# Performance work log

Hardware: AMD Instinct MI355X
Metric: run time of the kernel (lower is better)

Reference implementation:

```python
import jax, jax.numpy as jnp
import numpy as np

B = 131072   # batch (tokens)
D = 512      # d_model
P = 10       # n_programs
H = D // 4   # extractor hidden
MAXO = 4     # max operands
MAXR = 3     # max results


def setup_inputs() -> dict:
    key = jax.random.key(0)
    ks = jax.random.split(key, 6)
    hidden = jax.random.normal(ks[0], (B, D), jnp.float32)
    program_ids = jax.random.randint(ks[1], (B,), 0, P)
    Wr = jax.random.normal(ks[2], (D, P), jnp.float32) * (1.0 / np.sqrt(D))
    br = jnp.zeros((P,), jnp.float32)
    # stacked per-program extractor MLPs, output padded to MAXO (extra cols unused)
    W1 = jax.random.normal(ks[3], (P, D, H), jnp.float32) * (1.0 / np.sqrt(D))
    b1 = jnp.zeros((P, H), jnp.float32)
    W2 = jax.random.normal(ks[4], (P, H, MAXO), jnp.float32) * (1.0 / np.sqrt(H))
    b2 = jnp.zeros((P, MAXO), jnp.float32)
    return {"hidden": hidden, "program_ids": program_ids, "Wr": Wr, "br": br,
            "W1": W1, "b1": b1, "W2": W2, "b2": b2}


def _time_decompose(total_minutes):
    days = jnp.floor(total_minutes / 1440.0)
    rem = total_minutes - days * 1440.0
    hours = jnp.floor(rem / 60.0)
    minutes = rem - hours * 60.0
    return hours, minutes, days


def _safe(b):
    # avoid NaN/Inf from zero denominators in Mod/FloorDiv
    return jnp.where(b == 0, 1.0, b)


def _programs():
    # (fn -> tuple of result arrays, n_operands), order matches DEFAULT_PROGRAMS
    return [
        (lambda a, b: (a + b,), 2),                                   # IntAdd
        (lambda a, b: (a - b,), 2),                                   # IntSub
        (lambda a, b: (a * b,), 2),                                   # IntMul
        (lambda a, b: (jnp.mod(a, _safe(b)),), 2),                    # Mod
        (lambda a, b: (jnp.floor(a / _safe(b)),), 2),                 # FloorDiv
        (lambda h1, m1, h2, m2: _time_decompose(h1 * 60 + m1 + h2 * 60 + m2), 4),          # TimeAdd
        (lambda h1, m1, h2, m2: _time_decompose(h1 * 60 + m1 - (h2 * 60 + m2)), 4),        # TimeSub
        (lambda h1, m1, h2, m2: _time_decompose(jnp.abs(h1 * 60 + m1 - (h2 * 60 + m2))), 4),  # DurationBetween
        (lambda a, b: ((a > b).astype(jnp.float32),), 2),             # Greater
        (lambda a, b: ((a == b).astype(jnp.float32),), 2),            # Equal
    ]


def _compute_results(ops_rounded):
    # ops_rounded: [P, B, MAXO] -> results_all [P, B, MAXR]
    outs = []
    for idx, (fn, nop) in enumerate(_programs()):
        args = [ops_rounded[idx, :, i] for i in range(nop)]
        res = fn(*args)
        cols = list(res) + [jnp.zeros_like(res[0])] * (MAXR - len(res))
        outs.append(jnp.stack(cols, axis=-1))  # [B, MAXR]
    return jnp.stack(outs, axis=0)  # [P, B, MAXR]


def reference(hidden, program_ids, Wr, br, W1, b1, W2, b2):
    router_logits = hidden @ Wr + br                                  # [B, P]
    pre = jnp.einsum('bd,pdh->pbh', hidden, W1) + b1[:, None, :]      # [P, B, H]
    ops = jnp.einsum('pbh,pho->pbo', jax.nn.gelu(pre, approximate=False), W2) + b2[:, None, :]  # [P, B, MAXO]
    ops_rounded = jnp.round(ops)  # round_ste forward = round
    results_all = _compute_results(ops_rounded)                       # [P, B, MAXR]
    # combine: each row takes the result of its own program (masked scatter in torch)
    results = results_all[program_ids, jnp.arange(hidden.shape[0])]   # [B, MAXR]
    results = jax.lax.stop_gradient(results)  # torch .detach()
    return results, router_logits, ops, program_ids
```

## Files before the change

### kernel.cpp

```cpp
#include <hip/hip_runtime.h>
#include <math.h>

constexpr int D_   = 512;
constexpr int H_   = 128;
constexpr int P_   = 10;
constexpr int MAXO = 4;
constexpr int BM   = 128;
constexpr int BK   = 32;

typedef _Float16 f16;
typedef f16 f16x4 __attribute__((ext_vector_type(4)));
typedef f16 f16x8 __attribute__((ext_vector_type(8)));
typedef float f32x4 __attribute__((ext_vector_type(4)));

__device__ __forceinline__ float gelu_exact(float x) {
    return 0.5f * x * (1.0f + erff(x * 0.70710678118654752f));
}

__device__ __forceinline__ void time_decomp(float t, float& hr, float& mi, float& dy) {
    float days = floorf(t / 1440.0f);
    float rem  = t - days * 1440.0f;
    float hours = floorf(rem / 60.0f);
    float minutes = rem - hours * 60.0f;
    hr = hours; mi = minutes; dy = days;
}

__device__ __forceinline__ void g2l16(const f16* g, f16* l) {
    __builtin_amdgcn_global_load_lds(
        (const __attribute__((address_space(1))) void*)g,
        (__attribute__((address_space(3))) void*)l, 16, 0, 0);
}

__global__ __launch_bounds__(256) void cvt_w1_kernel(
    const float* __restrict__ W1, f16* __restrict__ hi, f16* __restrict__ lo)
{
    int i = blockIdx.x * 256 + threadIdx.x;
    float x = W1[i];
    f16 h = (f16)x;
    f16 L = (f16)(x - (float)h);
    int dh = i % (D_ * H_);
    int p  = i / (D_ * H_);
    int d  = dh / H_;
    int hh = dh % H_;
    size_t o = ((size_t)(p * H_ + hh)) * D_ + d;
    hi[o] = h; lo[o] = L;
}

template <bool WRITE_SPLIT>
__global__ __launch_bounds__(256) void router_cvt_kernel(
    const float* __restrict__ hidden, const float* __restrict__ Wr,
    const float* __restrict__ br, const int* __restrict__ pids,
    float* __restrict__ out_router, float* __restrict__ out_pids,
    f16* __restrict__ hidFhi, f16* __restrict__ hidFlo, int B)
{
    __shared__ float Wrs[D_ * 12];
    const int tid = threadIdx.x;
    for (int i = tid; i < D_ * P_; i += 256) {
        int k = i / P_;
        int q = i - k * P_;
        Wrs[k * 12 + q] = Wr[i];
    }
    __syncthreads();

    const int lane = tid & 63;
    const int wv   = tid >> 6;
    const int b    = blockIdx.x * 4 + wv;
    const float* hrow = hidden + (size_t)b * D_;
    const size_t t16  = (size_t)(b >> 4);
    const int    r15  = b & 15;

    float acc[P_];
#pragma unroll
    for (int q = 0; q < P_; ++q) acc[q] = 0.0f;

#pragma unroll
    for (int j = 0; j < 8; ++j) {
        int k = j * 64 + lane;
        float hv = hrow[k];
        if (WRITE_SPLIT) {
            int kc = k >> 5, l4k = (k >> 3) & 3, jj = k & 7;
            size_t off = ((t16 * 16 + kc) * 64 + l4k * 16 + r15) * 8 + jj;
            f16 hh = (f16)hv;
            hidFhi[off] = hh;
            hidFlo[off] = (f16)(hv - (float)hh);
        }
        float wv12[12];
        *reinterpret_cast<float4*>(&wv12[0]) = *reinterpret_cast<const float4*>(&Wrs[k * 12 + 0]);
        *reinterpret_cast<float4*>(&wv12[4]) = *reinterpret_cast<const float4*>(&Wrs[k * 12 + 4]);
        *reinterpret_cast<float2*>(&wv12[8]) = *reinterpret_cast<const float2*>(&Wrs[k * 12 + 8]);
#pragma unroll
        for (int q = 0; q < P_; ++q) acc[q] = fmaf(hv, wv12[q], acc[q]);
    }

#pragma unroll
    for (int off = 1; off < 64; off <<= 1) {
#pragma unroll
        for (int q = 0; q < P_; ++q)
            acc[q] += __shfl_xor(acc[q], off, 64);
    }

    if (lane == 0) {
        float* o = out_router + (size_t)b * P_;
#pragma unroll
        for (int q = 0; q < P_; ++q) o[q] = acc[q] + br[q];
        out_pids[b] = (float)pids[b];
    }
}

template <bool PRECONV>
__global__ __launch_bounds__(512, 2) void extractor_kernel(
    const float* __restrict__ hidden,
    const f16*   __restrict__ hidFhi,
    const f16*   __restrict__ hidFlo,
    const int*   __restrict__ pids,
    const f16*   __restrict__ W1Thi,
    const f16*   __restrict__ W1Tlo,
    const float* __restrict__ b1,
    const float* __restrict__ W2,
    const float* __restrict__ b2,
    float* __restrict__ out_results,
    float* __restrict__ out_ops,
    int B)
{
    __shared__ __align__(16) char smem[38912];
    float* red = (float*)(smem + 32768);
    float* W2s = (float*)(smem + 36864);

    const int bid = blockIdx.x;
    const int ngroups = gridDim.x / P_;
    int g, p;
    if ((ngroups & 7) == 0) {
        const int gpx = ngroups >> 3;
        const int x   = bid & 7;
        const int q   = bid >> 3;
        g = x * gpx + q / P_;
        p = q % P_;
    } else {
        g = bid / P_;
        p = bid % P_;
    }
    const int b0  = g * BM;
    const int tid = threadIdx.x;
    const int l   = tid & 63;
    const int w   = tid >> 6;
    const int wm  = w >> 1, wn = w & 1;
    const int l15 = l & 15, l4 = l >> 4;

    const int sg8 = (((l & 3) ^ ((l >> 3) & 3))) * 8;
    const int rd8 = ((l4 ^ ((l15 >> 1) & 3))) * 8;

    if (tid < H_) {
        ((f32x4*)W2s)[tid] = ((const f32x4*)(W2 + (size_t)p * H_ * 4))[tid];
    }

    f32x4 acc[2][4];
#pragma unroll
    for (int mi = 0; mi < 2; ++mi)
#pragma unroll
        for (int ni = 0; ni < 4; ++ni) acc[mi][ni] = (f32x4){0.f, 0.f, 0.f, 0.f};

    const f16* Bhig = W1Thi + (size_t)p * H_ * D_;
    const f16* Blog = W1Tlo + (size_t)p * H_ * D_;

    auto stageB = [&](int kc, char* buf) {
        f16* Bh = (f16*)(buf);
        f16* Bl = (f16*)(buf + 8192);
        const int r0 = w * 16;
        size_t gb = (size_t)(r0 + (l >> 2)) * D_ + kc * BK + sg8;
        g2l16(Bhig + gb, Bh + r0 * BK);
        g2l16(Blog + gb, Bl + r0 * BK);
    };

    auto loadA = [&](int kc, f16x8* aH, f16x8* aL) {
        if constexpr (PRECONV) {
#pragma unroll
            for (int mi = 0; mi < 2; ++mi) {
                const size_t off =
                    (((size_t)(b0 / 16 + wm * 2 + mi) * 16 + kc) * 64 + l) * 8;
                aH[mi] = *(const f16x8*)(hidFhi + off);
                aL[mi] = *(const f16x8*)(hidFlo + off);
            }
        }
    };

    auto compute = [&](const char* buf, const f16x8* aH, const f16x8* aL, int kc) {
        const f16* Bh = (const f16*)(buf);
        const f16* Bl = (const f16*)(buf + 8192);
        f16x8 bh[4], bl[4];
#pragma unroll
        for (int ni = 0; ni < 4; ++ni) {
            int hrow = wn * 64 + ni * 16 + l15;
            bh[ni] = *(const f16x8*)&Bh[hrow * BK + rd8];
            bl[ni] = *(const f16x8*)&Bl[hrow * BK + rd8];
        }
#pragma unroll
        for (int mi = 0; mi < 2; ++mi) {
            f16x8 a_h, a_l;
            if constexpr (PRECONV) {
                a_h = aH[mi]; a_l = aL[mi];
            } else {
                const float* rp = hidden + (size_t)(b0 + wm * 32 + mi * 16 + l15) * D_
                                 + kc * BK + l4 * 8;
                f32x4 x0 = *(const f32x4*)rp;
                f32x4 x1 = *(const f32x4*)(rp + 4);
#pragma unroll
                for (int j = 0; j < 4; ++j) {
                    f16 h0 = (f16)x0[j]; a_h[j] = h0; a_l[j] = (f16)(x0[j] - (float)h0);
                    f16 h1 = (f16)x1[j]; a_h[j + 4] = h1; a_l[j + 4] = (f16)(x1[j] - (float)h1);
                }
            }
#pragma unroll
            for (int ni = 0; ni < 4; ++ni) {
                acc[mi][ni] = __builtin_amdgcn_mfma_f32_16x16x32_f16(a_l, bh[ni], acc[mi][ni], 0, 0, 0);
                acc[mi][ni] = __builtin_amdgcn_mfma_f32_16x16x32_f16(a_h, bl[ni], acc[mi][ni], 0, 0, 0);
                acc[mi][ni] = __builtin_amdgcn_mfma_f32_16x16x32_f16(a_h, bh[ni], acc[mi][ni], 0, 0, 0);
            }
        }
    };

    char* buf0 = smem;
    char* buf1 = smem + 16384;
    f16x8 aHa[2], aLa[2], aHb[2], aLb[2];

    if constexpr (PRECONV) {
        loadA(0, aHa, aLa);
        stageB(0, buf0);
        asm volatile("s_waitcnt vmcnt(0)" ::: "memory");
        __builtin_amdgcn_s_barrier();
        for (int kc = 0; kc < 16; kc += 2) {
            loadA(kc + 1, aHb, aLb);
            stageB(kc + 1, buf1);
            asm volatile("s_waitcnt vmcnt(6)" ::: "memory");
            __builtin_amdgcn_s_barrier();
            compute(buf0, aHa, aLa, kc);
            __builtin_amdgcn_s_barrier();
            if (kc + 2 < 16) {
                loadA(kc + 2, aHa, aLa);
                stageB(kc + 2, buf0);
                asm volatile("s_waitcnt vmcnt(6)" ::: "memory");
            } else {
                asm volatile("s_waitcnt vmcnt(0)" ::: "memory");
            }
            __builtin_amdgcn_s_barrier();
            compute(buf1, aHb, aLb, kc + 1);
            __builtin_amdgcn_s_barrier();
        }
    } else {
        stageB(0, buf0);
        __syncthreads();
        for (int kc = 0; kc < 16; ++kc) {
            char* cur = (kc & 1) ? buf1 : buf0;
            char* nxt = (kc & 1) ? buf0 : buf1;
            if (kc < 15) stageB(kc + 1, nxt);
            compute(cur, aHa, aLa, kc);
            __syncthreads();
        }
    }

    float b1v[4];
#pragma unroll
    for (int ni = 0; ni < 4; ++ni)
        b1v[ni] = b1[p * H_ + wn * 64 + ni * 16 + l15];

#pragma unroll
    for (int mi = 0; mi < 2; ++mi) {
        float po[4][4];
#pragma unroll
        for (int r = 0; r < 4; ++r)
#pragma unroll
            for (int o = 0; o < 4; ++o) po[r][o] = 0.0f;

#pragma unroll
        for (int ni = 0; ni < 4; ++ni) {
            int h = wn * 64 + ni * 16 + l15;
            f32x4 w4 = ((const f32x4*)W2s)[h];
#pragma unroll
            for (int r = 0; r < 4; ++r) {
                float gg = gelu_exact(acc[mi][ni][r] + b1v[ni]);
#pragma unroll
                for (int o = 0; o < 4; ++o) po[r][o] = fmaf(gg, w4[o], po[r][o]);
            }
        }
#pragma unroll
        for (int off = 1; off < 16; off <<= 1) {
#pragma unroll
            for (int r = 0; r < 4; ++r)
#pragma unroll
                for (int o = 0; o < 4; ++o)
                    po[r][o] += __shfl_xor(po[r][o], off, 64);
        }
        float v = po[0][0];
#pragma unroll
        for (int rr = 0; rr < 4; ++rr)
#pragma unroll
            for (int oo = 0; oo < 4; ++oo)
                if (l15 == rr * 4 + oo) v = po[rr][oo];
        red[(wn * 128 + wm * 32 + mi * 16 + l4 * 4 + (l15 >> 2)) * 4 + (l15 & 3)] = v;
    }
    __syncthreads();

    if (tid < BM) {
        int b = b0 + tid;
        const float* r0p = &red[(0 * 128 + tid) * 4];
        const float* r1p = &red[(1 * 128 + tid) * 4];
        float o0 = r0p[0] + r1p[0] + b2[p * 4 + 0];
        float o1 = r0p[1] + r1p[1] + b2[p * 4 + 1];
        float o2 = r0p[2] + r1p[2] + b2[p * 4 + 2];
        float o3 = r0p[3] + r1p[3] + b2[p * 4 + 3];
        *reinterpret_cast<float4*>(out_ops + ((size_t)p * B + b) * MAXO) =
            make_float4(o0, o1, o2, o3);

        if (pids[b] == p) {
            float a0 = rintf(o0), a1 = rintf(o1), a2 = rintf(o2), a3 = rintf(o3);
            float r0 = 0.0f, r1 = 0.0f, r2 = 0.0f;
            switch (p) {
                case 0: r0 = a0 + a1; break;
                case 1: r0 = a0 - a1; break;
                case 2: r0 = a0 * a1; break;
                case 3: {
                    float bs = (a1 == 0.0f) ? 1.0f : a1;
                    float m = fmodf(a0, bs);
                    if (m != 0.0f && ((m < 0.0f) != (bs < 0.0f))) m += bs;
                    r0 = m;
                } break;
                case 4: {
                    float bs = (a1 == 0.0f) ? 1.0f : a1;
                    r0 = floorf(a0 / bs);
                } break;
                case 5: { float tt = a0 * 60.0f + a1 + a2 * 60.0f + a3; time_decomp(tt, r0, r1, r2); } break;
                case 6: { float tt = a0 * 60.0f + a1 - (a2 * 60.0f + a3); time_decomp(tt, r0, r1, r2); } break;
                case 7: { float tt = fabsf(a0 * 60.0f + a1 - (a2 * 60.0f + a3)); time_decomp(tt, r0, r1, r2); } break;
                case 8: r0 = (a0 > a1) ? 1.0f : 0.0f; break;
                case 9: r0 = (a0 == a1) ? 1.0f : 0.0f; break;
            }
            size_t ob = (size_t)b * 3;
            out_results[ob + 0] = r0;
            out_results[ob + 1] = r1;
            out_results[ob + 2] = r2;
        }
    }
}

extern "C" void kernel_launch(void* const* d_in, const int* in_sizes, int n_in,
                              void* d_out, int out_size, void* d_ws, size_t ws_size,
                              hipStream_t stream) {
    const float* hidden = (const float*)d_in[0];
    const int*   pids   = (const int*)  d_in[1];
    const float* Wr     = (const float*)d_in[2];
    const float* br     = (const float*)d_in[3];
    const float* W1     = (const float*)d_in[4];
    const float* b1     = (const float*)d_in[5];
    const float* W2     = (const float*)d_in[6];
    const float* b2     = (const float*)d_in[7];

    const int B = in_sizes[1];

    float* out         = (float*)d_out;
    float* out_results = out;
    float* out_router  = out + (size_t)B * 3;
    float* out_ops     = out + (size_t)B * 13;
    float* out_pids    = out + (size_t)B * 13 + (size_t)P_ * B * MAXO;

    const size_t nW1  = (size_t)P_ * H_ * D_;
    const size_t nHid = (size_t)B * D_;
    const size_t need = (2 * nW1 + 2 * nHid) * sizeof(f16);

    f16* W1Thi = (f16*)d_ws;
    f16* W1Tlo = W1Thi + nW1;

    cvt_w1_kernel<<<(int)(nW1 / 256), 256, 0, stream>>>(W1, W1Thi, W1Tlo);

    if (ws_size >= need) {
        f16* hidFhi = W1Tlo + nW1;
        f16* hidFlo = hidFhi + nHid;
        router_cvt_kernel<true><<<B / 4, 256, 0, stream>>>(
            hidden, Wr, br, pids, out_router, out_pids, hidFhi, hidFlo, B);
        extractor_kernel<true><<<(B / BM) * P_, 512, 0, stream>>>(
            hidden, hidFhi, hidFlo, pids, W1Thi, W1Tlo, b1, W2, b2,
            out_results, out_ops, B);
    } else {
        router_cvt_kernel<false><<<B / 4, 256, 0, stream>>>(
            hidden, Wr, br, pids, out_router, out_pids, nullptr, nullptr, B);
        extractor_kernel<false><<<(B / BM) * P_, 512, 0, stream>>>(
            hidden, nullptr, nullptr, pids, W1Thi, W1Tlo, b1, W2, b2,
            out_results, out_ops, B);
    }
}
```

Baseline: 791.2 us.

## Triple-buffer W1 LDS tiles with prefetch distance two in extractor GEMM

Expands shared memory to three B-tile buffers and restructures the preconverted main loop to stage W1 tiles two k-steps ahead while loading A fragments one step ahead. Each iteration now uses one wait/barrier pair instead of the previous two-phase double-buffer schedule, with vmcnt thresholds tuned to the outstanding loads. This aims to hide more global-load latency behind MFMA work. In exchange it uses more LDS per block, which could limit occupancy, and fully unrolls the loop, which adds code size.

```diff
diff --git a/kernel.cpp b/kernel.cpp
--- a/kernel.cpp
+++ b/kernel.cpp
@@ -122,9 +122,9 @@
     float* __restrict__ out_ops,
     int B)
 {
-    __shared__ __align__(16) char smem[38912];
-    float* red = (float*)(smem + 32768);
-    float* W2s = (float*)(smem + 36864);
+    __shared__ __align__(16) char smem[55296];
+    float* red = (float*)(smem + 49152);
+    float* W2s = (float*)(smem + 53248);
 
     const int bid = blockIdx.x;
     const int ngroups = gridDim.x / P_;
@@ -162,9 +162,9 @@
     const f16* Bhig = W1Thi + (size_t)p * H_ * D_;
     const f16* Blog = W1Tlo + (size_t)p * H_ * D_;
 
-    auto stageB = [&](int kc, char* buf) {
-        f16* Bh = (f16*)(buf);
-        f16* Bl = (f16*)(buf + 8192);
+    auto stageB = [&](int kc, int bi) {
+        f16* Bh = (f16*)(smem + bi * 16384);
+        f16* Bl = (f16*)(smem + bi * 16384 + 8192);
         const int r0 = w * 16;
         size_t gb = (size_t)(r0 + (l >> 2)) * D_ + kc * BK + sg8;
         g2l16(Bhig + gb, Bh + r0 * BK);
@@ -183,9 +183,9 @@
         }
     };
 
-    auto compute = [&](const char* buf, const f16x8* aH, const f16x8* aL, int kc) {
-        const f16* Bh = (const f16*)(buf);
-        const f16* Bl = (const f16*)(buf + 8192);
+    auto compute = [&](int bi, const f16x8* aH, const f16x8* aL, int kc) {
+        const f16* Bh = (const f16*)(smem + bi * 16384);
+        const f16* Bl = (const f16*)(smem + bi * 16384 + 8192);
         f16x8 bh[4], bl[4];
 #pragma unroll
         for (int ni = 0; ni < 4; ++ni) {
@@ -218,41 +218,33 @@
         }
     };
 
-    char* buf0 = smem;
-    char* buf1 = smem + 16384;
     f16x8 aHa[2], aLa[2], aHb[2], aLb[2];
 
     if constexpr (PRECONV) {
+        stageB(0, 0);
         loadA(0, aHa, aLa);
-        stageB(0, buf0);
-        asm volatile("s_waitcnt vmcnt(0)" ::: "memory");
-        __builtin_amdgcn_s_barrier();
-        for (int kc = 0; kc < 16; kc += 2) {
-            loadA(kc + 1, aHb, aLb);
-            stageB(kc + 1, buf1);
-            asm volatile("s_waitcnt vmcnt(6)" ::: "memory");
+        stageB(1, 1);
+#pragma unroll
+        for (int kc = 0; kc < 16; ++kc) {
+            if (kc + 1 < 16) {
+                if (kc & 1) loadA(kc + 1, aHa, aLa);
+                else        loadA(kc + 1, aHb, aLb);
+            }
+            if (kc + 2 < 16) stageB(kc + 2, (kc + 2) % 3);
+            if (kc <= 13)      asm volatile("s_waitcnt vmcnt(8)" ::: "memory");
+            else if (kc == 14) asm volatile("s_waitcnt vmcnt(6)" ::: "memory");
+            else               asm volatile("s_waitcnt vmcnt(0)" ::: "memory");
             __builtin_amdgcn_s_barrier();
-            compute(buf0, aHa, aLa, kc);
+            if (kc & 1) compute(kc % 3, aHb, aLb, kc);
+            else        compute(kc % 3, aHa, aLa, kc);
             __builtin_amdgcn_s_barrier();
-            if (kc + 2 < 16) {
-                loadA(kc + 2, aHa, aLa);
-                stageB(kc + 2, buf0);
-                asm volatile("s_waitcnt vmcnt(6)" ::: "memory");
-            } else {
-                asm volatile("s_waitcnt vmcnt(0)" ::: "memory");
-            }
-            __builtin_amdgcn_s_barrier();
-            compute(buf1, aHb, aLb, kc + 1);
-            __builtin_amdgcn_s_barrier();
         }
     } else {
-        stageB(0, buf0);
+        stageB(0, 0);
         __syncthreads();
         for (int kc = 0; kc < 16; ++kc) {
-            char* cur = (kc & 1) ? buf1 : buf0;
-            char* nxt = (kc & 1) ? buf0 : buf1;
-            if (kc < 15) stageB(kc + 1, nxt);
-            compute(cur, aHa, aLa, kc);
+            if (kc < 15) stageB(kc + 1, (kc + 1) & 1);
+            compute(kc & 1, aHa, aLa, kc);
             __syncthreads();
         }
     }
```

After: 781.4 us. No clear change (-1.2%).
